# Kernel tuning notes

Measured on AMD Instinct MI355X. Metric: run time of the kernel, lower is better.

The kernel has to match this reference:

```python
import jax, jax.numpy as jnp
import numpy as np

ALPHA = 16.0
RANK = 64
SCALING = ALPHA / RANK


def setup_inputs() -> dict:
    key = jax.random.key(0)
    k1, k2, k3, k4, k5 = jax.random.split(key, 5)
    B, S, DIN, DOUT = 4, 4096, 4096, 4096
    x = jax.random.normal(k1, (B, S, DIN), dtype=jnp.float32)
    lora_A = jax.random.normal(k2, (RANK, DIN), dtype=jnp.float32) / np.sqrt(DIN)
    lora_B = jax.random.normal(k3, (DOUT, RANK), dtype=jnp.float32)
    lora_A_scale = jax.random.uniform(k4, (RANK,), dtype=jnp.float32, minval=0.5, maxval=1.5)
    lora_B_scale = jax.random.uniform(k5, (DOUT,), dtype=jnp.float32, minval=0.5, maxval=1.5)
    return {"x": x, "lora_A": lora_A, "lora_B": lora_B,
            "lora_A_scale": lora_A_scale, "lora_B_scale": lora_B_scale}


def reference(x, lora_A, lora_B, lora_A_scale, lora_B_scale):
    # INT8 dequant path: quantized.float() * scale.unsqueeze(-1)
    A_dq = lora_A * lora_A_scale[:, None]          # [rank, in]
    B_dq = lora_B * lora_B_scale[:, None]          # [out, rank]
    # x @ A.T -> [B, S, rank]; then @ B.T -> [B, S, out]; final scaling
    h = jnp.einsum('bsi,ri->bsr', x, A_dq)
    out = jnp.einsum('bsr,or->bso', h, B_dq)
    return out * SCALING
```

## Files before the change

kernel.cpp:

```cpp
#include <hip/hip_runtime.h>


#define M_TOTAL 16384
#define DIN     4096
#define DOUT    4096
#define RANK    64

typedef __bf16 bf16_8 __attribute__((ext_vector_type(8)));
typedef __bf16 bf16_4 __attribute__((ext_vector_type(4)));
typedef float  f32x4  __attribute__((ext_vector_type(4)));

__global__ __launch_bounds__(256) void prep_kernel(
    const float* __restrict__ A, const float* __restrict__ Bm,
    const float* __restrict__ sA, const float* __restrict__ sB,
    __bf16* __restrict__ Abf, __bf16* __restrict__ Bbf) {
  int i = (blockIdx.x * 256 + threadIdx.x) * 4;
  float4 a = *(const float4*)(A + i);
  float sa = sA[i >> 12];
  bf16_4 va;
  va[0] = (__bf16)(a.x * sa); va[1] = (__bf16)(a.y * sa);
  va[2] = (__bf16)(a.z * sa); va[3] = (__bf16)(a.w * sa);
  *(bf16_4*)(Abf + i) = va;

  float4 b = *(const float4*)(Bm + i);
  float sb = sB[i >> 6] * 0.25f;
  bf16_4 vb;
  vb[0] = (__bf16)(b.x * sb); vb[1] = (__bf16)(b.y * sb);
  vb[2] = (__bf16)(b.z * sb); vb[3] = (__bf16)(b.w * sb);
  *(bf16_4*)(Bbf + i) = vb;
}

__global__ __launch_bounds__(256, 2) void gemm1_kernel(
    const float* __restrict__ x, const __bf16* __restrict__ Abf,
    __bf16* __restrict__ h) {
  __shared__ __bf16 xs[32 * 72];
  __shared__ __bf16 as[64 * 72];

  const int t = threadIdx.x;
  const int mBase = blockIdx.x * 32;

  const int xrow = t >> 3;
  const int xc   = t & 7;
  const float* xg = x + (size_t)(mBase + xrow) * DIN + xc * 4;

  const int arow = t >> 2;
  const int ac   = t & 3;
  const __bf16* ag = Abf + (size_t)arow * DIN + ac * 8;

  const int lane = t & 63;
  const int w    = t >> 6;
  const int mt   = w >> 1;
  const int nh   = w & 1;
  const int lr   = lane & 15;
  const int quad = lane >> 4;

  f32x4 acc0 = {0.f, 0.f, 0.f, 0.f};
  f32x4 acc1 = {0.f, 0.f, 0.f, 0.f};

  float4 f0 = *(const float4*)(xg);
  float4 f1 = *(const float4*)(xg + 32);
  bf16_8 a0 = *(const bf16_8*)(ag);
  bf16_8 a1 = *(const bf16_8*)(ag + 32);

  for (int k0 = 0; k0 < DIN; k0 += 64) {
    __syncthreads();

    bf16_4 v;
    v[0] = (__bf16)f0.x; v[1] = (__bf16)f0.y;
    v[2] = (__bf16)f0.z; v[3] = (__bf16)f0.w;
    *(bf16_4*)&xs[xrow * 72 + xc * 4] = v;
    v[0] = (__bf16)f1.x; v[1] = (__bf16)f1.y;
    v[2] = (__bf16)f1.z; v[3] = (__bf16)f1.w;
    *(bf16_4*)&xs[xrow * 72 + xc * 4 + 32] = v;
    *(bf16_8*)&as[arow * 72 + ac * 8] = a0;
    *(bf16_8*)&as[arow * 72 + ac * 8 + 32] = a1;

    __syncthreads();

    if (k0 + 64 < DIN) {
      f0 = *(const float4*)(xg + (k0 + 64));
      f1 = *(const float4*)(xg + (k0 + 64) + 32);
      a0 = *(const bf16_8*)(ag + (k0 + 64));
      a1 = *(const bf16_8*)(ag + (k0 + 64) + 32);
    }

#pragma unroll
    for (int ks = 0; ks < 2; ++ks) {
      bf16_8 af  = *(const bf16_8*)&xs[(mt * 16 + lr) * 72 + ks * 32 + quad * 8];
      bf16_8 bf0 = *(const bf16_8*)&as[(nh * 32 + lr) * 72 + ks * 32 + quad * 8];
      bf16_8 bf1 = *(const bf16_8*)&as[(nh * 32 + 16 + lr) * 72 + ks * 32 + quad * 8];
      acc0 = __builtin_amdgcn_mfma_f32_16x16x32_bf16(af, bf0, acc0, 0, 0, 0);
      acc1 = __builtin_amdgcn_mfma_f32_16x16x32_bf16(af, bf1, acc1, 0, 0, 0);
    }
  }

  const int m = mBase + mt * 16 + quad * 4;
  const int n = nh * 32 + lr;
#pragma unroll
  for (int i = 0; i < 4; ++i) {
    h[(size_t)(m + i) * RANK + n]      = (__bf16)acc0[i];
    h[(size_t)(m + i) * RANK + n + 16] = (__bf16)acc1[i];
  }
}

__global__ __launch_bounds__(256, 4) void gemm2_kernel(
    const __bf16* __restrict__ h, const __bf16* __restrict__ Bbf,
    float* __restrict__ out) {
  __shared__ __bf16 hs[128 * 72];
  __shared__ __bf16 bs[128 * 72];

  const int t = threadIdx.x;
  const int mBase = blockIdx.y * 128;
  const int nBase = blockIdx.x * 128;

  {
    const __bf16* hg = h   + (size_t)mBase * RANK;
    const __bf16* bg = Bbf + (size_t)nBase * RANK;
#pragma unroll
    for (int l = 0; l < 4; ++l) {
      int q = l * 2048 + t * 8;
      bf16_8 hv = *(const bf16_8*)(hg + q);
      bf16_8 bv = *(const bf16_8*)(bg + q);
      int row = q >> 6;
      int col = q & 63;
      *(bf16_8*)&hs[row * 72 + col] = hv;
      *(bf16_8*)&bs[row * 72 + col] = bv;
    }
  }
  __syncthreads();

  const int lane = t & 63;
  const int w    = t >> 6;
  const int wm   = w >> 1;
  const int wn   = w & 1;
  const int lr   = lane & 15;
  const int quad = lane >> 4;

  f32x4 acc[4][4];
#pragma unroll
  for (int mt = 0; mt < 4; ++mt)
#pragma unroll
    for (int nt = 0; nt < 4; ++nt)
      acc[mt][nt] = (f32x4){0.f, 0.f, 0.f, 0.f};

#pragma unroll
  for (int ks = 0; ks < 2; ++ks) {
    bf16_8 af[4], bfr[4];
#pragma unroll
    for (int mt = 0; mt < 4; ++mt)
      af[mt] = *(const bf16_8*)&hs[(wm * 64 + mt * 16 + lr) * 72 + ks * 32 + quad * 8];
#pragma unroll
    for (int nt = 0; nt < 4; ++nt)
      bfr[nt] = *(const bf16_8*)&bs[(wn * 64 + nt * 16 + lr) * 72 + ks * 32 + quad * 8];
#pragma unroll
    for (int mt = 0; mt < 4; ++mt)
#pragma unroll
      for (int nt = 0; nt < 4; ++nt)
        acc[mt][nt] = __builtin_amdgcn_mfma_f32_16x16x32_bf16(af[mt], bfr[nt], acc[mt][nt], 0, 0, 0);
  }

#pragma unroll
  for (int mt = 0; mt < 4; ++mt) {
    int m = mBase + wm * 64 + mt * 16 + quad * 4;
#pragma unroll
    for (int nt = 0; nt < 4; ++nt) {
      int n = nBase + wn * 64 + nt * 16 + lr;
#pragma unroll
      for (int i = 0; i < 4; ++i)
        out[(size_t)(m + i) * DOUT + n] = acc[mt][nt][i];
    }
  }
}

extern "C" void kernel_launch(void* const* d_in, const int* in_sizes, int n_in,
                              void* d_out, int out_size, void* d_ws, size_t ws_size,
                              hipStream_t stream) {
  const float* x  = (const float*)d_in[0];
  const float* A  = (const float*)d_in[1];
  const float* Bm = (const float*)d_in[2];
  const float* sA = (const float*)d_in[3];
  const float* sB = (const float*)d_in[4];
  float* out = (float*)d_out;

  __bf16* Abf = (__bf16*)d_ws;
  __bf16* Bbf = Abf + (size_t)RANK * DIN;
  __bf16* h   = Bbf + (size_t)DOUT * RANK;

  prep_kernel<<<256, 256, 0, stream>>>(A, Bm, sA, sB, Abf, Bbf);
  gemm1_kernel<<<M_TOTAL / 32, 256, 0, stream>>>(x, Abf, h);
  gemm2_kernel<<<dim3(DOUT / 128, M_TOTAL / 128), 256, 0, stream>>>(h, Bbf, out);
}
```

Before: 475.8 us.

## Fuse both LoRA GEMMs into one kernel with split-K waves and direct register operands

Replaces the separate down-projection and up-projection kernels with one fused kernel per 16-row tile. Each of the four waves computes a quarter of the K range of x·Aᵀ, loading operands straight from global memory into MFMA registers without LDS staging. The partial sums are reduced through shared memory into h, which is then multiplied by B to write the full 4096-wide output row block. This removes the h round trip through global memory and a kernel launch, and stores the output with 16-byte vector writes instead of scalar ones. In exchange, A and B are reread by every block (they should mostly stay in cache), and the x loads per lane are narrow, strided row reads.

```diff
diff --git a/kernel.cpp b/kernel.cpp
--- a/kernel.cpp
+++ b/kernel.cpp
@@ -30,145 +30,92 @@
   *(bf16_4*)(Bbf + i) = vb;
 }
 
-__global__ __launch_bounds__(256, 2) void gemm1_kernel(
+__global__ __launch_bounds__(256, 4) void lora_kernel(
     const float* __restrict__ x, const __bf16* __restrict__ Abf,
-    __bf16* __restrict__ h) {
-  __shared__ __bf16 xs[32 * 72];
-  __shared__ __bf16 as[64 * 72];
+    const __bf16* __restrict__ Bbf, float* __restrict__ out) {
+  __shared__ alignas(16) float  part[4 * 1024];
+  __shared__ alignas(16) __bf16 hs[16 * RANK];
 
-  const int t = threadIdx.x;
-  const int mBase = blockIdx.x * 32;
-
-  const int xrow = t >> 3;
-  const int xc   = t & 7;
-  const float* xg = x + (size_t)(mBase + xrow) * DIN + xc * 4;
-
-  const int arow = t >> 2;
-  const int ac   = t & 3;
-  const __bf16* ag = Abf + (size_t)arow * DIN + ac * 8;
-
+  const int t    = threadIdx.x;
   const int lane = t & 63;
   const int w    = t >> 6;
-  const int mt   = w >> 1;
-  const int nh   = w & 1;
   const int lr   = lane & 15;
   const int quad = lane >> 4;
+  const int mBase = blockIdx.x * 16;
 
-  f32x4 acc0 = {0.f, 0.f, 0.f, 0.f};
-  f32x4 acc1 = {0.f, 0.f, 0.f, 0.f};
+  const float*  xg = x   + (size_t)(mBase + lr) * DIN + w * 1024 + quad * 8;
+  const __bf16* ag = Abf + (size_t)lr * DIN           + w * 1024 + quad * 8;
+
+  f32x4 acc0 = {0.f,0.f,0.f,0.f};
+  f32x4 acc1 = {0.f,0.f,0.f,0.f};
+  f32x4 acc2 = {0.f,0.f,0.f,0.f};
+  f32x4 acc3 = {0.f,0.f,0.f,0.f};
 
   float4 f0 = *(const float4*)(xg);
-  float4 f1 = *(const float4*)(xg + 32);
+  float4 f1 = *(const float4*)(xg + 4);
   bf16_8 a0 = *(const bf16_8*)(ag);
-  bf16_8 a1 = *(const bf16_8*)(ag + 32);
+  bf16_8 a1 = *(const bf16_8*)(ag + 16 * DIN);
+  bf16_8 a2 = *(const bf16_8*)(ag + 32 * DIN);
+  bf16_8 a3 = *(const bf16_8*)(ag + 48 * DIN);
 
-  for (int k0 = 0; k0 < DIN; k0 += 64) {
-    __syncthreads();
-
-    bf16_4 v;
-    v[0] = (__bf16)f0.x; v[1] = (__bf16)f0.y;
-    v[2] = (__bf16)f0.z; v[3] = (__bf16)f0.w;
-    *(bf16_4*)&xs[xrow * 72 + xc * 4] = v;
-    v[0] = (__bf16)f1.x; v[1] = (__bf16)f1.y;
-    v[2] = (__bf16)f1.z; v[3] = (__bf16)f1.w;
-    *(bf16_4*)&xs[xrow * 72 + xc * 4 + 32] = v;
-    *(bf16_8*)&as[arow * 72 + ac * 8] = a0;
-    *(bf16_8*)&as[arow * 72 + ac * 8 + 32] = a1;
-
-    __syncthreads();
-
-    if (k0 + 64 < DIN) {
-      f0 = *(const float4*)(xg + (k0 + 64));
-      f1 = *(const float4*)(xg + (k0 + 64) + 32);
-      a0 = *(const bf16_8*)(ag + (k0 + 64));
-      a1 = *(const bf16_8*)(ag + (k0 + 64) + 32);
+  for (int k = 32; k <= 1024; k += 32) {
+    float4 g0 = f0, g1 = f1;
+    bf16_8 c0 = a0, c1 = a1, c2 = a2, c3 = a3;
+    if (k < 1024) {
+      f0 = *(const float4*)(xg + k);
+      f1 = *(const float4*)(xg + k + 4);
+      a0 = *(const bf16_8*)(ag + k);
+      a1 = *(const bf16_8*)(ag + k + 16 * DIN);
+      a2 = *(const bf16_8*)(ag + k + 32 * DIN);
+      a3 = *(const bf16_8*)(ag + k + 48 * DIN);
     }
-
-#pragma unroll
-    for (int ks = 0; ks < 2; ++ks) {
-      bf16_8 af  = *(const bf16_8*)&xs[(mt * 16 + lr) * 72 + ks * 32 + quad * 8];
-      bf16_8 bf0 = *(const bf16_8*)&as[(nh * 32 + lr) * 72 + ks * 32 + quad * 8];
-      bf16_8 bf1 = *(const bf16_8*)&as[(nh * 32 + 16 + lr) * 72 + ks * 32 + quad * 8];
-      acc0 = __builtin_amdgcn_mfma_f32_16x16x32_bf16(af, bf0, acc0, 0, 0, 0);
-      acc1 = __builtin_amdgcn_mfma_f32_16x16x32_bf16(af, bf1, acc1, 0, 0, 0);
-    }
+    bf16_8 xv;
+    xv[0] = (__bf16)g0.x; xv[1] = (__bf16)g0.y;
+    xv[2] = (__bf16)g0.z; xv[3] = (__bf16)g0.w;
+    xv[4] = (__bf16)g1.x; xv[5] = (__bf16)g1.y;
+    xv[6] = (__bf16)g1.z; xv[7] = (__bf16)g1.w;
+    acc0 = __builtin_amdgcn_mfma_f32_16x16x32_bf16(xv, c0, acc0, 0, 0, 0);
+    acc1 = __builtin_amdgcn_mfma_f32_16x16x32_bf16(xv, c1, acc1, 0, 0, 0);
+    acc2 = __builtin_amdgcn_mfma_f32_16x16x32_bf16(xv, c2, acc2, 0, 0, 0);
+    acc3 = __builtin_amdgcn_mfma_f32_16x16x32_bf16(xv, c3, acc3, 0, 0, 0);
   }
 
-  const int m = mBase + mt * 16 + quad * 4;
-  const int n = nh * 32 + lr;
+  {
+    float* pw = part + w * 1024;
 #pragma unroll
-  for (int i = 0; i < 4; ++i) {
-    h[(size_t)(m + i) * RANK + n]      = (__bf16)acc0[i];
-    h[(size_t)(m + i) * RANK + n + 16] = (__bf16)acc1[i];
-  }
-}
-
-__global__ __launch_bounds__(256, 4) void gemm2_kernel(
-    const __bf16* __restrict__ h, const __bf16* __restrict__ Bbf,
-    float* __restrict__ out) {
-  __shared__ __bf16 hs[128 * 72];
-  __shared__ __bf16 bs[128 * 72];
-
-  const int t = threadIdx.x;
-  const int mBase = blockIdx.y * 128;
-  const int nBase = blockIdx.x * 128;
-
-  {
-    const __bf16* hg = h   + (size_t)mBase * RANK;
-    const __bf16* bg = Bbf + (size_t)nBase * RANK;
-#pragma unroll
-    for (int l = 0; l < 4; ++l) {
-      int q = l * 2048 + t * 8;
-      bf16_8 hv = *(const bf16_8*)(hg + q);
-      bf16_8 bv = *(const bf16_8*)(bg + q);
-      int row = q >> 6;
-      int col = q & 63;
-      *(bf16_8*)&hs[row * 72 + col] = hv;
-      *(bf16_8*)&bs[row * 72 + col] = bv;
+    for (int i = 0; i < 4; ++i) {
+      pw[(quad * 4 + i) * 64 +      lr] = acc0[i];
+      pw[(quad * 4 + i) * 64 + 16 + lr] = acc1[i];
+      pw[(quad * 4 + i) * 64 + 32 + lr] = acc2[i];
+      pw[(quad * 4 + i) * 64 + 48 + lr] = acc3[i];
     }
   }
   __syncthreads();
 
-  const int lane = t & 63;
-  const int w    = t >> 6;
-  const int wm   = w >> 1;
-  const int wn   = w & 1;
-  const int lr   = lane & 15;
-  const int quad = lane >> 4;
+  {
+    const f32x4* pp = (const f32x4*)part;
+    f32x4 s = pp[t] + pp[t + 256] + pp[t + 512] + pp[t + 768];
+    bf16_4 hv;
+    hv[0] = (__bf16)s[0]; hv[1] = (__bf16)s[1];
+    hv[2] = (__bf16)s[2]; hv[3] = (__bf16)s[3];
+    ((bf16_4*)hs)[t] = hv;
+  }
+  __syncthreads();
 
-  f32x4 acc[4][4];
-#pragma unroll
-  for (int mt = 0; mt < 4; ++mt)
-#pragma unroll
-    for (int nt = 0; nt < 4; ++nt)
-      acc[mt][nt] = (f32x4){0.f, 0.f, 0.f, 0.f};
+  bf16_8 hf0 = *(const bf16_8*)&hs[lr * RANK + quad * 8];
+  bf16_8 hf1 = *(const bf16_8*)&hs[lr * RANK + 32 + quad * 8];
 
-#pragma unroll
-  for (int ks = 0; ks < 2; ++ks) {
-    bf16_8 af[4], bfr[4];
-#pragma unroll
-    for (int mt = 0; mt < 4; ++mt)
-      af[mt] = *(const bf16_8*)&hs[(wm * 64 + mt * 16 + lr) * 72 + ks * 32 + quad * 8];
-#pragma unroll
-    for (int nt = 0; nt < 4; ++nt)
-      bfr[nt] = *(const bf16_8*)&bs[(wn * 64 + nt * 16 + lr) * 72 + ks * 32 + quad * 8];
-#pragma unroll
-    for (int mt = 0; mt < 4; ++mt)
-#pragma unroll
-      for (int nt = 0; nt < 4; ++nt)
-        acc[mt][nt] = __builtin_amdgcn_mfma_f32_16x16x32_bf16(af[mt], bfr[nt], acc[mt][nt], 0, 0, 0);
-  }
+  const __bf16* bg = Bbf + (size_t)(w * 1024 + lr) * RANK + quad * 8;
+  float* og = out + (size_t)(mBase + lr) * DOUT + w * 1024;
 
-#pragma unroll
-  for (int mt = 0; mt < 4; ++mt) {
-    int m = mBase + wm * 64 + mt * 16 + quad * 4;
-#pragma unroll
-    for (int nt = 0; nt < 4; ++nt) {
-      int n = nBase + wn * 64 + nt * 16 + lr;
-#pragma unroll
-      for (int i = 0; i < 4; ++i)
-        out[(size_t)(m + i) * DOUT + n] = acc[mt][nt][i];
-    }
+#pragma unroll 4
+  for (int nt = 0; nt < 64; ++nt) {
+    bf16_8 b0 = *(const bf16_8*)(bg + nt * 16 * RANK);
+    bf16_8 b1 = *(const bf16_8*)(bg + nt * 16 * RANK + 32);
+    f32x4 o = {0.f, 0.f, 0.f, 0.f};
+    o = __builtin_amdgcn_mfma_f32_16x16x32_bf16(b0, hf0, o, 0, 0, 0);
+    o = __builtin_amdgcn_mfma_f32_16x16x32_bf16(b1, hf1, o, 0, 0, 0);
+    *(f32x4*)(og + nt * 16 + quad * 4) = o;
   }
 }
 
@@ -184,9 +131,7 @@
 
   __bf16* Abf = (__bf16*)d_ws;
   __bf16* Bbf = Abf + (size_t)RANK * DIN;
-  __bf16* h   = Bbf + (size_t)DOUT * RANK;
 
   prep_kernel<<<256, 256, 0, stream>>>(A, Bm, sA, sB, Abf, Bbf);
-  gemm1_kernel<<<M_TOTAL / 32, 256, 0, stream>>>(x, Abf, h);
-  gemm2_kernel<<<dim3(DOUT / 128, M_TOTAL / 128), 256, 0, stream>>>(h, Bbf, out);
+  lora_kernel<<<M_TOTAL / 16, 256, 0, stream>>>(x, Abf, Bbf, out);
 }
```

After: 549.1 us. 15.4% more time.
